# Kernel tuning notes

Hardware: AMD Instinct MI355X
Metric: run time of the kernel (lower is better)

## Reference

```python
import jax, jax.numpy as jnp
import numpy as np

B, T, E = 4, 2048, 1024
NUM_HEADS = 16
HEAD_SIZE = E // NUM_HEADS


def _rope_tables(T, E):
    # thetas over pairs, repeat_interleave by 2 -> shape (E,)
    thetas = 10000.0 ** (-jnp.arange(0, E, 2, dtype=jnp.float32) / E)
    thetas = jnp.repeat(thetas, 2)
    angles = jnp.arange(T, dtype=jnp.float32)[:, None] * thetas[None, :]  # (T, E)
    return jnp.sin(angles), jnp.cos(angles)


def _rotate(x, sin, cos):
    # x: (B, T, E); pairs (x0, x1) -> (-x1, x0)
    Bx, Tx, Ex = x.shape
    xp = x.reshape(Bx, Tx, Ex // 2, 2)
    rot = jnp.stack([-xp[..., 1], xp[..., 0]], axis=-1).reshape(Bx, Tx, Ex)
    return x * cos + rot * sin


def setup_inputs() -> dict:
    key = jax.random.key(0)
    ks = jax.random.split(key, 6)
    scale = 1.0 / np.sqrt(E)
    return {
        "input": jax.random.normal(ks[0], (B, T, E), dtype=jnp.float32),
        "Wq": jax.random.normal(ks[1], (E, E), dtype=jnp.float32) * scale,
        "Wk": jax.random.normal(ks[2], (E, E), dtype=jnp.float32) * scale,
        "Wv": jax.random.normal(ks[3], (E, E), dtype=jnp.float32) * scale,
        "Wo": jax.random.normal(ks[4], (E, E), dtype=jnp.float32) * scale,
        "bo": jnp.zeros((E,), dtype=jnp.float32),
    }


def reference(input, Wq, Wk, Wv, Wo, bo):
    Bx, Tx, Ex = input.shape
    sin, cos = _rope_tables(Tx, Ex)
    rx = _rotate(input, sin, cos)
    q = rx @ Wq.T
    k = rx @ Wk.T
    v = input @ Wv.T
    # (B, H, T, hd)
    def split_heads(t):
        return t.reshape(Bx, Tx, NUM_HEADS, HEAD_SIZE).transpose(0, 2, 1, 3)
    q, k, v = split_heads(q), split_heads(k), split_heads(v)
    scores = jnp.einsum("bhqd,bhkd->bhqk", q, k)
    causal = jnp.tril(jnp.ones((Tx, Tx), dtype=bool))
    scores = jnp.where(causal[None, None], scores, -jnp.inf) / np.sqrt(HEAD_SIZE)
    attn = jax.nn.softmax(scores, axis=-1)  # dropout omitted (eval mode)
    out = jnp.einsum("bhqk,bhkd->bhqd", attn, v)
    out = out.transpose(0, 2, 1, 3).reshape(Bx, Tx, Ex)
    return out @ Wo.T + bo
```

## Files before the change

kernel.cpp:

```cpp
#include <hip/hip_runtime.h>

typedef unsigned short u16;
typedef unsigned int   u32;
typedef __attribute__((ext_vector_type(4))) float f32x4;
typedef __attribute__((ext_vector_type(8))) __bf16 bf16x8;
typedef __attribute__((ext_vector_type(2))) u32  u32x2;
typedef __attribute__((ext_vector_type(4))) u32  u32x4;

#define LDS_CAST(p) ((__attribute__((address_space(3))) void*)(p))
#define GLB_CAST(p) ((const __attribute__((address_space(1))) void*)(p))

__device__ __forceinline__ void load_lds16(const void* g, void* l) {
    __builtin_amdgcn_global_load_lds(GLB_CAST(g), LDS_CAST(l), 16, 0, 0);
}

__device__ __forceinline__ u32 lds_off(const void* p) {
    return (u32)(size_t)(const __attribute__((address_space(3))) void*)p;
}

__device__ __forceinline__ u16 f2bf(float f) {
    union { float f; u32 u; } v; v.f = f;
    u32 r = (v.u + 0x7FFFu + ((v.u >> 16) & 1u)) >> 16;
    return (u16)r;
}

__global__ __launch_bounds__(256) void rope_cast(const float* __restrict__ x,
                                                 u16* __restrict__ xb,
                                                 u16* __restrict__ rxb) {
    int idx = blockIdx.x * 256 + threadIdx.x;
    int e2 = (idx & 511) * 2;
    int t  = (idx >> 9) & 2047;
    float2 v = *(const float2*)&x[(size_t)idx * 2];
    float theta = expf(-0.0089944730194981f * (float)e2);
    float angle = (float)t * theta;
    float sa, ca;
    sincosf(angle, &sa, &ca);
    float r0 = v.x * ca - v.y * sa;
    float r1 = v.y * ca + v.x * sa;
    u32 xp  = (u32)f2bf(v.x) | ((u32)f2bf(v.y) << 16);
    u32 rxp = (u32)f2bf(r0)  | ((u32)f2bf(r1)  << 16);
    *(u32*)&xb[(size_t)idx * 2]  = xp;
    *(u32*)&rxb[(size_t)idx * 2] = rxp;
}

__global__ __launch_bounds__(256) void wcast(const float* __restrict__ a,
                                             const float* __restrict__ b,
                                             const float* __restrict__ c,
                                             const float* __restrict__ d,
                                             u16* __restrict__ out) {
    int i = blockIdx.x * 256 + threadIdx.x;
    int w = i >> 20, j = i & 1048575;
    float v = (w == 0) ? a[j] : (w == 1) ? b[j] : (w == 2) ? c[j] : d[j];
    out[i] = f2bf(v);
}

template <int MODE>
__global__ __launch_bounds__(256) void gemm128(const u16* __restrict__ A,
                                               const u16* __restrict__ W,
                                               u16* __restrict__ outb,
                                               float* __restrict__ outf,
                                               const float* __restrict__ bias) {
    constexpr int Kd = 1024, Nd = 1024;
    __shared__ u16 As[128 * 64];
    __shared__ u16 Bs[128 * 64];
    const int tid = threadIdx.x;
    const int m0 = blockIdx.x * 128;
    const int n0 = blockIdx.y * 128;
    const int wid = tid >> 6, lane = tid & 63;
    const int wr = wid >> 1, wc = wid & 1;
    const int lr = lane & 15, lhi = lane >> 4;

    f32x4 acc[4][4] = {};

    for (int k0 = 0; k0 < Kd; k0 += 64) {
        if (k0) __syncthreads();
#pragma unroll
        for (int i = 0; i < 4; ++i) {
            int cidx = tid + 256 * i;
            int row = cidx >> 3, col = (cidx & 7) * 8;
            load_lds16(A + (size_t)(m0 + row) * Kd + k0 + col, &As[row * 64 + col]);
        }
#pragma unroll
        for (int i = 0; i < 4; ++i) {
            int cidx = tid + 256 * i;
            int row = cidx >> 3, col = (cidx & 7) * 8;
            load_lds16(W + (size_t)(n0 + row) * Kd + k0 + col, &Bs[row * 64 + col]);
        }
        __syncthreads();
#pragma unroll
        for (int c = 0; c < 2; ++c) {
            bf16x8 a[4], b[4];
#pragma unroll
            for (int m = 0; m < 4; ++m)
                a[m] = *(const bf16x8*)&As[(wr * 64 + m * 16 + lr) * 64 + c * 32 + lhi * 8];
#pragma unroll
            for (int n = 0; n < 4; ++n)
                b[n] = *(const bf16x8*)&Bs[(wc * 64 + n * 16 + lr) * 64 + c * 32 + lhi * 8];
#pragma unroll
            for (int m = 0; m < 4; ++m)
#pragma unroll
                for (int n = 0; n < 4; ++n)
                    acc[m][n] = __builtin_amdgcn_mfma_f32_16x16x32_bf16(a[m], b[n], acc[m][n], 0, 0, 0);
        }
    }

#pragma unroll
    for (int m = 0; m < 4; ++m) {
        int rowb = m0 + wr * 64 + m * 16 + lhi * 4;
#pragma unroll
        for (int n = 0; n < 4; ++n) {
            int col = n0 + wc * 64 + n * 16 + lr;
#pragma unroll
            for (int r = 0; r < 4; ++r) {
                int mg = rowb + r;
                float v = acc[m][n][r];
                if (MODE == 0) {
                    int bb = mg >> 11, t = mg & 2047;
                    int h = col >> 6, d = col & 63;
                    outb[((((size_t)bb * 16 + h) * 2048) + t) * 64 + d] = f2bf(v);
                } else {
                    outf[(size_t)mg * Nd + col] = v + bias[col];
                }
            }
        }
    }
}

__device__ __forceinline__ void attn_pass(const bf16x8 (&qa)[2], f32x4 (&acc)[4],
                                          float (&m_i)[4], float (&l_i)[4],
                                          const u16* ks, const u16* vcur, u32 vsb,
                                          u16* pw, int lr, int lhi,
                                          int kv0, int q0w, bool diag, bool use_tr) {
    f32x4 s4[4] = {};
    __builtin_amdgcn_s_setprio(1);
#pragma unroll
    for (int c = 0; c < 2; ++c)
#pragma unroll
        for (int n = 0; n < 4; ++n) {
            int r = n * 16 + lr;
            bf16x8 kb = *(const bf16x8*)&ks[r * 64 + ((c * 32 + lhi * 8) ^ ((r & 7) * 8))];
            s4[n] = __builtin_amdgcn_mfma_f32_16x16x32_bf16(qa[c], kb, s4[n], 0, 0, 0);
        }
    __builtin_amdgcn_s_setprio(0);

    if (diag) {
#pragma unroll
        for (int n = 0; n < 4; ++n) {
            int kvg = kv0 + n * 16 + lr;
#pragma unroll
            for (int r = 0; r < 4; ++r)
                if (kvg > q0w + lhi * 4 + r) s4[n][r] = -1e30f;
        }
    }

    float mx[4] = { -1e30f, -1e30f, -1e30f, -1e30f };
#pragma unroll
    for (int n = 0; n < 4; ++n)
#pragma unroll
        for (int r = 0; r < 4; ++r) mx[r] = fmaxf(mx[r], s4[n][r]);
#pragma unroll
    for (int off = 8; off; off >>= 1)
#pragma unroll
        for (int r = 0; r < 4; ++r) mx[r] = fmaxf(mx[r], __shfl_xor(mx[r], off));

    float rs[4] = { 0.f, 0.f, 0.f, 0.f };
#pragma unroll
    for (int r = 0; r < 4; ++r) {
        float mnew = fmaxf(m_i[r], mx[r]);
        float sc = __expf(m_i[r] - mnew);
        m_i[r] = mnew;
        l_i[r] *= sc;
#pragma unroll
        for (int nd = 0; nd < 4; ++nd) acc[nd][r] *= sc;
    }
#pragma unroll
    for (int n = 0; n < 4; ++n)
#pragma unroll
        for (int r = 0; r < 4; ++r) {
            float pv = __expf(s4[n][r] - m_i[r]);
            rs[r] += pv;
            int qloc = lhi * 4 + r;
            pw[qloc * 64 + ((n * 16 + lr) ^ ((qloc & 7) * 8))] = f2bf(pv);
        }
#pragma unroll
    for (int off = 8; off; off >>= 1)
#pragma unroll
        for (int r = 0; r < 4; ++r) rs[r] += __shfl_xor(rs[r], off);
#pragma unroll
    for (int r = 0; r < 4; ++r) l_i[r] += rs[r];

    __builtin_amdgcn_s_setprio(1);
#pragma unroll
    for (int c = 0; c < 2; ++c) {
        bf16x8 pa = *(const bf16x8*)&pw[lr * 64 + ((c * 32 + lhi * 8) ^ ((lr & 7) * 8))];
        union { bf16x8 v; u32 w[4]; u16 h[8]; } vb[4];
        if (use_tr) {
            u32x2 lo[4], hi[4];
#pragma unroll
            for (int nd = 0; nd < 4; ++nd) {
                u32 a = vsb + (u32)((c * 32 + lhi * 8 + nd) * 128 + lr * 2);
                asm volatile("ds_read_b64_tr_b16 %0, %2\n\t"
                             "ds_read_b64_tr_b16 %1, %2 offset:512"
                             : "=&v"(lo[nd]), "=&v"(hi[nd]) : "v"(a));
            }
            asm volatile("s_waitcnt lgkmcnt(0)" ::: "memory");
            __builtin_amdgcn_sched_barrier(0);
#pragma unroll
            for (int nd = 0; nd < 4; ++nd) {
                vb[nd].w[0] = lo[nd].x; vb[nd].w[1] = lo[nd].y;
                vb[nd].w[2] = hi[nd].x; vb[nd].w[3] = hi[nd].y;
            }
        } else {
#pragma unroll
            for (int nd = 0; nd < 4; ++nd)
#pragma unroll
                for (int i = 0; i < 8; ++i) {
                    int k = c * 32 + lhi * 8 + i;
                    vb[nd].h[i] = vcur[((k >> 2) << 8) + (nd << 6) + ((k & 3) << 4) + lr];
                }
        }
#pragma unroll
        for (int nd = 0; nd < 4; ++nd)
            acc[nd] = __builtin_amdgcn_mfma_f32_16x16x32_bf16(pa, vb[nd].v, acc[nd], 0, 0, 0);
    }
    __builtin_amdgcn_s_setprio(0);
}

__global__ __launch_bounds__(256) void attn64(const u16* __restrict__ Q,
                                              const u16* __restrict__ K,
                                              const u16* __restrict__ V,
                                              u16* __restrict__ O) {
    constexpr int T = 2048;
    __shared__ u16 Ks[2][64 * 64];
    __shared__ u16 Vs[2][64 * 64];
    __shared__ u16 Ps[4][16 * 64];
    const int tid = threadIdx.x, wid = tid >> 6, lane = tid & 63;
    const int lr = lane & 15, lhi = lane >> 4;
    const int bh = blockIdx.y;
    const int qtA = blockIdx.x;
    const int qtB = 31 - qtA;
    const int q0wA = qtA * 64 + wid * 16;
    const int q0wB = qtB * 64 + wid * 16;
    const size_t base = (size_t)bh * T * 64;
    const u16* Qp = Q + base;
    const u16* Kp = K + base;
    const u16* Vp = V + base;

    bf16x8 qaA[2], qaB[2];
#pragma unroll
    for (int c = 0; c < 2; ++c) {
        bf16x8 tA = *(const bf16x8*)&Qp[(size_t)(q0wA + lr) * 64 + c * 32 + lhi * 8];
        bf16x8 tB = *(const bf16x8*)&Qp[(size_t)(q0wB + lr) * 64 + c * 32 + lhi * 8];
        bf16x8 oA, oB;
#pragma unroll
        for (int i = 0; i < 8; ++i) {
            oA[i] = (__bf16)((float)tA[i] * 0.125f);
            oB[i] = (__bf16)((float)tB[i] * 0.125f);
        }
        qaA[c] = oA; qaB[c] = oB;
    }

    f32x4 accA[4] = {}, accB[4] = {};
    float m_iA[4], l_iA[4], m_iB[4], l_iB[4];
#pragma unroll
    for (int r = 0; r < 4; ++r) {
        m_iA[r] = -1e30f; l_iA[r] = 0.f;
        m_iB[r] = -1e30f; l_iB[r] = 0.f;
    }

    {
        u16* vt = (u16*)&Vs[0][0];
#pragma unroll
        for (int j = 0; j < 16; ++j) vt[tid * 16 + j] = (u16)(tid * 16 + j);
    }
    __syncthreads();
    bool use_tr;
    {
        const u32 vsb0 = lds_off(&Vs[0][0]);
        bool ok = true;
#pragma unroll
        for (int t = 0; t < 2; ++t) {
            const int c = t ? 1 : 0, nd = t ? 3 : 0;
            u32 a = vsb0 + (u32)((c * 32 + lhi * 8 + nd) * 128 + lr * 2);
            u32x2 lo, hi;
            asm volatile("ds_read_b64_tr_b16 %0, %2\n\t"
                         "ds_read_b64_tr_b16 %1, %2 offset:512"
                         : "=&v"(lo), "=&v"(hi) : "v"(a));
            asm volatile("s_waitcnt lgkmcnt(0)" ::: "memory");
            __builtin_amdgcn_sched_barrier(0);
            union { u32 w[4]; u16 h[8]; } u;
            u.w[0] = lo.x; u.w[1] = lo.y; u.w[2] = hi.x; u.w[3] = hi.y;
#pragma unroll
            for (int i = 0; i < 8; ++i) {
                int k = c * 32 + lhi * 8 + i;
                int e = ((k >> 2) << 8) + (nd << 6) + ((k & 3) << 4) + lr;
                ok = ok && (u.h[i] == (u16)e);
            }
        }
        use_tr = (bool)__all((int)ok);
    }
    __syncthreads();

#define STAGE(bb, kv0s)                                                          \
    {                                                                            \
        _Pragma("unroll")                                                        \
        for (int i = 0; i < 2; ++i) {                                            \
            int q = tid + 256 * i;                                               \
            int krow = q >> 3;                                                   \
            int kcol = ((q & 7) ^ (krow & 7)) * 8;                               \
            load_lds16(Kp + (size_t)((kv0s) + krow) * 64 + kcol, &Ks[bb][q * 8]);\
            int vk = ((q >> 5) << 2) + ((q >> 1) & 3);                           \
            int vd = (((q >> 3) & 3) << 4) + ((q & 1) << 3);                     \
            load_lds16(Vp + (size_t)((kv0s) + vk) * 64 + vd, &Vs[bb][q * 8]);    \
        }                                                                        \
    }

    STAGE(0, 0);
    __syncthreads();

    u16* pw = Ps[wid];
    int buf = 0;
    for (int kt = 0; kt <= qtB; ++kt) {
        const int kv0 = kt * 64;
        if (kt < qtB) STAGE(buf ^ 1, kv0 + 64);

        const u16* ks = Ks[buf];
        const u16* vcur = Vs[buf];
        const u32 vsb = lds_off(vcur);

        if (kt <= qtA)
            attn_pass(qaA, accA, m_iA, l_iA, ks, vcur, vsb, pw, lr, lhi,
                      kv0, q0wA, kt == qtA, use_tr);
        attn_pass(qaB, accB, m_iB, l_iB, ks, vcur, vsb, pw, lr, lhi,
                  kv0, q0wB, kt == qtB, use_tr);

        __syncthreads();
        buf ^= 1;
    }
#undef STAGE

    const int b = bh >> 4, h = bh & 15;
#pragma unroll
    for (int nd = 0; nd < 4; ++nd)
#pragma unroll
        for (int r = 0; r < 4; ++r) {
            int d = h * 64 + nd * 16 + lr;
            int qgA = q0wA + lhi * 4 + r;
            int qgB = q0wB + lhi * 4 + r;
            O[(size_t)(b * 2048 + qgA) * 1024 + d] = f2bf(accA[nd][r] / l_iA[r]);
            O[(size_t)(b * 2048 + qgB) * 1024 + d] = f2bf(accB[nd][r] / l_iB[r]);
        }
}

extern "C" void kernel_launch(void* const* d_in, const int* in_sizes, int n_in,
                              void* d_out, int out_size, void* d_ws, size_t ws_size,
                              hipStream_t stream) {
    const float* x  = (const float*)d_in[0];
    const float* Wq = (const float*)d_in[1];
    const float* Wk = (const float*)d_in[2];
    const float* Wv = (const float*)d_in[3];
    const float* Wo = (const float*)d_in[4];
    const float* bo = (const float*)d_in[5];

    char* ws = (char*)d_ws;
    u16* Wqb = (u16*)ws;
    u16* Wkb = Wqb + (1 << 20);
    u16* Wvb = Wkb + (1 << 20);
    u16* Wob = Wvb + (1 << 20);
    u16* xb  = (u16*)(ws + (size_t)8 * 1024 * 1024);
    u16* rxb = xb  + (size_t)8388608;
    u16* Qb  = rxb + (size_t)8388608;
    u16* Kb  = Qb  + (size_t)8388608;
    u16* Vb  = Kb  + (size_t)8388608;
    u16* Ob  = Vb  + (size_t)8388608;

    rope_cast<<<16384, 256, 0, stream>>>(x, xb, rxb);
    wcast<<<16384, 256, 0, stream>>>(Wq, Wk, Wv, Wo, Wqb);

    dim3 g(64, 8);
    gemm128<0><<<g, 256, 0, stream>>>(rxb, Wqb, Qb, nullptr, nullptr);
    gemm128<0><<<g, 256, 0, stream>>>(rxb, Wkb, Kb, nullptr, nullptr);
    gemm128<0><<<g, 256, 0, stream>>>(xb,  Wvb, Vb, nullptr, nullptr);

    attn64<<<dim3(16, 64), 256, 0, stream>>>(Qb, Kb, Vb, Ob);

    gemm128<1><<<g, 256, 0, stream>>>(Ob, Wob, nullptr, (float*)d_out, bo);
}
```

Before: 386.2 us.

## Fuse QKV projections into one launch and streamline attention softmax P path

Merges the three Q/K/V projection GEMMs into a single 64x24 grid launch that picks its input (rope-rotated or plain x) by output column range and writes to contiguous Q/K/V buffers. In attention, the softmax scale is folded with log2(e) into Q so exp2 can be used directly. P is stored transposed with packed 64-bit writes and read back through ds_read_b64_tr_b16 instead of scalar swizzled stores. Manual bf16 rounding is replaced with hardware conversion. This cuts launch overhead, tail effects and LDS store count, at the cost of an extra lgkmcnt wait and possible rounding differences.

```diff
diff --git a/kernel.cpp b/kernel.cpp
--- a/kernel.cpp
+++ b/kernel.cpp
@@ -22,6 +22,21 @@
     union { float f; u32 u; } v; v.f = f;
     u32 r = (v.u + 0x7FFFu + ((v.u >> 16) & 1u)) >> 16;
     return (u16)r;
+}
+
+__device__ __forceinline__ u16 bfc(float f) {
+    return __builtin_bit_cast(u16, (__bf16)f);
+}
+__device__ __forceinline__ u32 pack_bf16(float a, float b) {
+    return (u32)bfc(a) | ((u32)bfc(b) << 16);
+}
+
+__device__ __forceinline__ float exp2fast(float x) {
+#if __has_builtin(__builtin_amdgcn_exp2f)
+    return __builtin_amdgcn_exp2f(x);
+#else
+    return __expf(x * 0.6931471805599453f);
+#endif
 }
 
 __global__ __launch_bounds__(256) void rope_cast(const float* __restrict__ x,
@@ -55,17 +70,19 @@
 }
 
 template <int MODE>
-__global__ __launch_bounds__(256) void gemm128(const u16* __restrict__ A,
+__global__ __launch_bounds__(256) void gemm128(const u16* __restrict__ A0,
+                                               const u16* __restrict__ A1,
                                                const u16* __restrict__ W,
                                                u16* __restrict__ outb,
                                                float* __restrict__ outf,
                                                const float* __restrict__ bias) {
-    constexpr int Kd = 1024, Nd = 1024;
+    constexpr int Kd = 1024;
     __shared__ u16 As[128 * 64];
     __shared__ u16 Bs[128 * 64];
     const int tid = threadIdx.x;
     const int m0 = blockIdx.x * 128;
     const int n0 = blockIdx.y * 128;
+    const u16* A = (MODE == 0 && n0 >= 2048) ? A1 : A0;
     const int wid = tid >> 6, lane = tid & 63;
     const int wr = wid >> 1, wc = wid & 1;
     const int lr = lane & 15, lhi = lane >> 4;
@@ -116,10 +133,11 @@
                 float v = acc[m][n][r];
                 if (MODE == 0) {
                     int bb = mg >> 11, t = mg & 2047;
-                    int h = col >> 6, d = col & 63;
-                    outb[((((size_t)bb * 16 + h) * 2048) + t) * 64 + d] = f2bf(v);
+                    int hg = col >> 6, d = col & 63;
+                    outb[(size_t)(hg >> 4) * 8388608 +
+                         (((size_t)(bb * 16 + (hg & 15)) * 2048) + t) * 64 + d] = bfc(v);
                 } else {
-                    outf[(size_t)mg * Nd + col] = v + bias[col];
+                    outf[(size_t)mg * 1024 + col] = v + bias[col];
                 }
             }
         }
@@ -129,7 +147,7 @@
 __device__ __forceinline__ void attn_pass(const bf16x8 (&qa)[2], f32x4 (&acc)[4],
                                           float (&m_i)[4], float (&l_i)[4],
                                           const u16* ks, const u16* vcur, u32 vsb,
-                                          u16* pw, int lr, int lhi,
+                                          u16* pw, u32 ptb, int lr, int lhi,
                                           int kv0, int q0w, bool diag, bool use_tr) {
     f32x4 s4[4] = {};
     __builtin_amdgcn_s_setprio(1);
@@ -163,25 +181,26 @@
 #pragma unroll
         for (int r = 0; r < 4; ++r) mx[r] = fmaxf(mx[r], __shfl_xor(mx[r], off));
 
-    float rs[4] = { 0.f, 0.f, 0.f, 0.f };
 #pragma unroll
     for (int r = 0; r < 4; ++r) {
         float mnew = fmaxf(m_i[r], mx[r]);
-        float sc = __expf(m_i[r] - mnew);
+        float sc = exp2fast(m_i[r] - mnew);
         m_i[r] = mnew;
         l_i[r] *= sc;
 #pragma unroll
         for (int nd = 0; nd < 4; ++nd) acc[nd][r] *= sc;
     }
-#pragma unroll
-    for (int n = 0; n < 4; ++n)
-#pragma unroll
-        for (int r = 0; r < 4; ++r) {
-            float pv = __expf(s4[n][r] - m_i[r]);
-            rs[r] += pv;
-            int qloc = lhi * 4 + r;
-            pw[qloc * 64 + ((n * 16 + lr) ^ ((qloc & 7) * 8))] = f2bf(pv);
-        }
+    float rs[4] = { 0.f, 0.f, 0.f, 0.f };
+#pragma unroll
+    for (int n = 0; n < 4; ++n) {
+        float p0 = exp2fast(s4[n][0] - m_i[0]);
+        float p1 = exp2fast(s4[n][1] - m_i[1]);
+        float p2 = exp2fast(s4[n][2] - m_i[2]);
+        float p3 = exp2fast(s4[n][3] - m_i[3]);
+        rs[0] += p0; rs[1] += p1; rs[2] += p2; rs[3] += p3;
+        u32x2 wv; wv.x = pack_bf16(p0, p1); wv.y = pack_bf16(p2, p3);
+        *(u32x2*)&pw[(n * 16 + lr) * 16 + lhi * 4] = wv;
+    }
 #pragma unroll
     for (int off = 8; off; off >>= 1)
 #pragma unroll
@@ -189,12 +208,19 @@
 #pragma unroll
     for (int r = 0; r < 4; ++r) l_i[r] += rs[r];
 
+    asm volatile("s_waitcnt lgkmcnt(0)" ::: "memory");
+
     __builtin_amdgcn_s_setprio(1);
 #pragma unroll
     for (int c = 0; c < 2; ++c) {
-        bf16x8 pa = *(const bf16x8*)&pw[lr * 64 + ((c * 32 + lhi * 8) ^ ((lr & 7) * 8))];
+        union { bf16x8 v; u32 w[4]; u16 h[8]; } pa;
         union { bf16x8 v; u32 w[4]; u16 h[8]; } vb[4];
         if (use_tr) {
+            u32x2 plo, phi;
+            u32 paddr = ptb + (u32)(c * 1024 + lhi * 256 + lr * 2);
+            asm volatile("ds_read_b64_tr_b16 %0, %2\n\t"
+                         "ds_read_b64_tr_b16 %1, %2 offset:128"
+                         : "=&v"(plo), "=&v"(phi) : "v"(paddr));
             u32x2 lo[4], hi[4];
 #pragma unroll
             for (int nd = 0; nd < 4; ++nd) {
@@ -205,6 +231,7 @@
             }
             asm volatile("s_waitcnt lgkmcnt(0)" ::: "memory");
             __builtin_amdgcn_sched_barrier(0);
+            pa.w[0] = plo.x; pa.w[1] = plo.y; pa.w[2] = phi.x; pa.w[3] = phi.y;
 #pragma unroll
             for (int nd = 0; nd < 4; ++nd) {
                 vb[nd].w[0] = lo[nd].x; vb[nd].w[1] = lo[nd].y;
@@ -212,16 +239,17 @@
             }
         } else {
 #pragma unroll
-            for (int nd = 0; nd < 4; ++nd)
-#pragma unroll
-                for (int i = 0; i < 8; ++i) {
-                    int k = c * 32 + lhi * 8 + i;
+            for (int i = 0; i < 8; ++i) {
+                int k = c * 32 + lhi * 8 + i;
+                pa.h[i] = pw[k * 16 + lr];
+#pragma unroll
+                for (int nd = 0; nd < 4; ++nd)
                     vb[nd].h[i] = vcur[((k >> 2) << 8) + (nd << 6) + ((k & 3) << 4) + lr];
-                }
+            }
         }
 #pragma unroll
         for (int nd = 0; nd < 4; ++nd)
-            acc[nd] = __builtin_amdgcn_mfma_f32_16x16x32_bf16(pa, vb[nd].v, acc[nd], 0, 0, 0);
+            acc[nd] = __builtin_amdgcn_mfma_f32_16x16x32_bf16(pa.v, vb[nd].v, acc[nd], 0, 0, 0);
     }
     __builtin_amdgcn_s_setprio(0);
 }
@@ -233,7 +261,7 @@
     constexpr int T = 2048;
     __shared__ u16 Ks[2][64 * 64];
     __shared__ u16 Vs[2][64 * 64];
-    __shared__ u16 Ps[4][16 * 64];
+    __shared__ u16 Ps[4][64 * 16];
     const int tid = threadIdx.x, wid = tid >> 6, lane = tid & 63;
     const int lr = lane & 15, lhi = lane >> 4;
     const int bh = blockIdx.y;
@@ -246,6 +274,7 @@
     const u16* Kp = K + base;
     const u16* Vp = V + base;
 
+    const float QS = 0.18033688011112042f;
     bf16x8 qaA[2], qaB[2];
 #pragma unroll
     for (int c = 0; c < 2; ++c) {
@@ -254,8 +283,8 @@
         bf16x8 oA, oB;
 #pragma unroll
         for (int i = 0; i < 8; ++i) {
-            oA[i] = (__bf16)((float)tA[i] * 0.125f);
-            oB[i] = (__bf16)((float)tB[i] * 0.125f);
+            oA[i] = (__bf16)((float)tA[i] * QS);
+            oB[i] = (__bf16)((float)tB[i] * QS);
         }
         qaA[c] = oA; qaB[c] = oB;
     }
@@ -319,6 +348,7 @@
     __syncthreads();
 
     u16* pw = Ps[wid];
+    const u32 ptb = lds_off(pw);
     int buf = 0;
     for (int kt = 0; kt <= qtB; ++kt) {
         const int kv0 = kt * 64;
@@ -329,9 +359,9 @@
         const u32 vsb = lds_off(vcur);
 
         if (kt <= qtA)
-            attn_pass(qaA, accA, m_iA, l_iA, ks, vcur, vsb, pw, lr, lhi,
+            attn_pass(qaA, accA, m_iA, l_iA, ks, vcur, vsb, pw, ptb, lr, lhi,
                       kv0, q0wA, kt == qtA, use_tr);
-        attn_pass(qaB, accB, m_iB, l_iB, ks, vcur, vsb, pw, lr, lhi,
+        attn_pass(qaB, accB, m_iB, l_iB, ks, vcur, vsb, pw, ptb, lr, lhi,
                   kv0, q0wB, kt == qtB, use_tr);
 
         __syncthreads();
@@ -347,8 +377,8 @@
             int d = h * 64 + nd * 16 + lr;
             int qgA = q0wA + lhi * 4 + r;
             int qgB = q0wB + lhi * 4 + r;
-            O[(size_t)(b * 2048 + qgA) * 1024 + d] = f2bf(accA[nd][r] / l_iA[r]);
-            O[(size_t)(b * 2048 + qgB) * 1024 + d] = f2bf(accB[nd][r] / l_iB[r]);
+            O[(size_t)(b * 2048 + qgA) * 1024 + d] = bfc(accA[nd][r] / l_iA[r]);
+            O[(size_t)(b * 2048 + qgB) * 1024 + d] = bfc(accB[nd][r] / l_iB[r]);
         }
 }
 
@@ -364,9 +394,7 @@
 
     char* ws = (char*)d_ws;
     u16* Wqb = (u16*)ws;
-    u16* Wkb = Wqb + (1 << 20);
-    u16* Wvb = Wkb + (1 << 20);
-    u16* Wob = Wvb + (1 << 20);
+    u16* Wob = Wqb + 3 * (1 << 20);
     u16* xb  = (u16*)(ws + (size_t)8 * 1024 * 1024);
     u16* rxb = xb  + (size_t)8388608;
     u16* Qb  = rxb + (size_t)8388608;
@@ -377,12 +405,9 @@
     rope_cast<<<16384, 256, 0, stream>>>(x, xb, rxb);
     wcast<<<16384, 256, 0, stream>>>(Wq, Wk, Wv, Wo, Wqb);
 
-    dim3 g(64, 8);
-    gemm128<0><<<g, 256, 0, stream>>>(rxb, Wqb, Qb, nullptr, nullptr);
-    gemm128<0><<<g, 256, 0, stream>>>(rxb, Wkb, Kb, nullptr, nullptr);
-    gemm128<0><<<g, 256, 0, stream>>>(xb,  Wvb, Vb, nullptr, nullptr);
+    gemm128<0><<<dim3(64, 24), 256, 0, stream>>>(rxb, xb, Wqb, Qb, nullptr, nullptr);
 
     attn64<<<dim3(16, 64), 256, 0, stream>>>(Qb, Kb, Vb, Ob);
 
-    gemm128<1><<<g, 256, 0, stream>>>(Ob, Wob, nullptr, (float*)d_out, bo);
-}
+    gemm128<1><<<dim3(64, 8), 256, 0, stream>>>(Ob, Ob, Wob, nullptr, (float*)d_out, bo);
+}
```

Result: faster. 372.8 us (-3.5%).
